# Kernel optimization log

Measured on AMD Instinct MI355X. Metric: run time of the kernel, lower is better.

Reference implementation:

```python
import jax, jax.numpy as jnp
import numpy as np

V = 1_000_000
D = 128
H = 128
DO = 128
S = 50_000


def setup_inputs() -> dict:
    key = jax.random.key(0)
    k1, k2, k3, k4, k5 = jax.random.split(key, 5)
    element_embeddings = jax.random.normal(k1, (V, D), dtype=jnp.float32)
    element_to_sample_map = jnp.sort(jax.random.randint(k2, (V,), 0, S))
    W_key = jax.random.normal(k3, (H, D), dtype=jnp.float32) * 0.05
    W_value = jax.random.normal(k4, (H, D), dtype=jnp.float32) * 0.05
    W_out = jax.random.normal(k5, (DO, D), dtype=jnp.float32) * 0.05
    return {
        "element_embeddings": element_embeddings,
        "element_to_sample_map": element_to_sample_map,
        "num_samples": S,
        "W_key": W_key,
        "W_value": W_value,
        "W_out": W_out,
    }


def _segment_log_softmax(scores, seg, num_segments):
    # numerically stable per-segment log-softmax (eps=0 as in original)
    m = jax.ops.segment_max(scores, seg, num_segments=num_segments)  # [S]
    m = jnp.where(jnp.isfinite(m), m, 0.0)  # guard empty segments
    shifted = scores - m[seg]
    sum_exp = jax.ops.segment_sum(jnp.exp(shifted), seg, num_segments=num_segments)  # [S]
    lse = jnp.log(sum_exp)
    return shifted - lse[seg]


def reference(element_embeddings, element_to_sample_map, num_samples, W_key, W_value, W_out):
    seg = element_to_sample_map
    # key summarizer: linear projection then per-sample mean (SimpleVarSizedElementReduce 'mean')
    proj = element_embeddings @ W_key.T  # [V, H]
    seg_sum = jax.ops.segment_sum(proj, seg, num_segments=num_samples)  # [S, H]
    counts = jax.ops.segment_sum(jnp.ones((proj.shape[0],), proj.dtype), seg, num_segments=num_samples)
    keys = seg_sum / jnp.maximum(counts, 1.0)[:, None]  # [S, H]

    keys_all = keys[seg]  # gather [V, H]
    values = element_embeddings @ W_value.T  # [V, H]
    attention_scores = jnp.einsum("vh,vh->v", keys_all, values)  # [V]
    attention_probs = jnp.exp(_segment_log_softmax(attention_scores, seg, num_samples))  # [V]

    out_vals = (element_embeddings @ W_out.T) * attention_probs[:, None]  # [V, DO]
    return jax.ops.segment_sum(out_vals, seg, num_segments=num_samples)  # [S, DO]
```

## Files before the change

### kernel.cpp

```cpp
#include <hip/hip_runtime.h>
#include <math.h>

#define G    4
#define CAP  104

typedef __attribute__((ext_vector_type(8))) short bf16x8;
typedef __attribute__((ext_vector_type(4))) float f32x4;

__global__ void k_segstarts(const int* __restrict__ map, int* __restrict__ starts,
                            int V, int S) {
    int i = blockIdx.x * blockDim.x + threadIdx.x;
    if (i >= V) return;
    int cur  = map[i];
    int prev = (i == 0) ? -1 : map[i - 1];
    for (int s = prev + 1; s <= cur; ++s) starts[s] = i;
    if (i == V - 1) {
        for (int s = cur + 1; s <= S; ++s) starts[s] = V;
    }
}

__device__ __forceinline__ unsigned f2bf_rte(float x) {
    unsigned b = __float_as_uint(x);
    b += 0x7FFFu + ((b >> 16) & 1u);
    return b >> 16;
}
__device__ __forceinline__ float bfu_lo(unsigned u) {
    return __uint_as_float(u << 16);
}
__device__ __forceinline__ float bfu_hi(unsigned u) {
    return __uint_as_float(u & 0xFFFF0000u);
}

template <int CTRL>
__device__ __forceinline__ float dpp_add(float v) {
    int t = __builtin_amdgcn_update_dpp(0, __float_as_int(v), CTRL, 0xF, 0xF, true);
    return v + __int_as_float(t);
}
__device__ __forceinline__ float red32_sum(float v) {
    v = dpp_add<0xB1>(v);
    v = dpp_add<0x4E>(v);
    v = dpp_add<0x141>(v);
    v = dpp_add<0x140>(v);
    v += __int_as_float(__builtin_amdgcn_ds_swizzle(__float_as_int(v), 0x401F));
    return v;
}

__global__ void k_prep(const float* __restrict__ Wk, const float* __restrict__ Wv,
                       const float* __restrict__ Wo,
                       unsigned short* __restrict__ Mpk,
                       unsigned short* __restrict__ Wpk) {
    const int i = blockIdx.x;
    const int j = threadIdx.x;
    float acc = 0.f;
#pragma unroll 8
    for (int h = 0; h < 128; ++h)
        acc += Wk[h * 128 + i] * Wv[h * 128 + j];
    acc *= 1.4426950408889634f;

    const int kt  = i >> 5;
    const int kg  = (i >> 3) & 3;
    const int t   = i & 7;
    const int jt  = j >> 4;
    const int l16 = j & 15;
    const int lane = kg * 16 + l16;
    const size_t idx = ((size_t)(kt * 8 + jt) * 64 + lane) * 8 + t;
    Mpk[idx] = (unsigned short)f2bf_rte(acc);
    Wpk[idx] = (unsigned short)f2bf_rte(Wo[j * 128 + i]);
}

__device__ __forceinline__ bf16x8 pack_a8(const float* p) {
    union { unsigned u[4]; bf16x8 v; } r;
    const float4 f0 = *(const float4*)p;
    const float4 f1 = *(const float4*)(p + 4);
    r.u[0] = (__float_as_uint(f0.y) & 0xFFFF0000u) | (__float_as_uint(f0.x) >> 16);
    r.u[1] = (__float_as_uint(f0.w) & 0xFFFF0000u) | (__float_as_uint(f0.z) >> 16);
    r.u[2] = (__float_as_uint(f1.y) & 0xFFFF0000u) | (__float_as_uint(f1.x) >> 16);
    r.u[3] = (__float_as_uint(f1.w) & 0xFFFF0000u) | (__float_as_uint(f1.z) >> 16);
    return r.v;
}

__global__ __launch_bounds__(256, 4) void k_main(
    const float* __restrict__ E, const int* __restrict__ starts,
    const unsigned short* __restrict__ Mpk, const unsigned short* __restrict__ Wpk,
    float* __restrict__ out, int V, int S)
{
    __shared__ unsigned sA[CAP][64];
    __shared__ float    sE[G][128];
    __shared__ float    sQ[G][128];

    const int tid  = threadIdx.x;
    const int w    = tid >> 6;
    const int lane = tid & 63;
    const int s0   = blockIdx.x * G;

    const int se    = min(s0 + G, S);
    const int gr0   = starts[s0];
    const int nrows = starts[se] - gr0;
    const bool staged = (nrows <= CAP);

    const int c  = lane & 31;
    const int g  = lane >> 5;

    if (staged && nrows > 0) {
        const int q4 = tid & 31;
        const int rr = tid >> 5;
        const float* gp = E + (size_t)gr0 * 128 + q4 * 4;
#pragma unroll
        for (int b = 0; b < 3; ++b) {
            const int nb = (b == 2) ? 3 : 5;
            const int k0 = b * 5;
            float4 t[5];
            for (int k = 0; k < nb; ++k) {
                const int r = min(rr + (k0 + k) * 8, nrows - 1);
                t[k] = *(const float4*)(gp + (size_t)r * 128);
            }
            for (int k = 0; k < nb; ++k) {
                uint2 u;
                u.x = f2bf_rte(t[k].x) | (f2bf_rte(t[k].y) << 16);
                u.y = f2bf_rte(t[k].z) | (f2bf_rte(t[k].w) << 16);
                *(uint2*)&sA[rr + (k0 + k) * 8][q4 * 2] = u;
            }
        }
    }
    __syncthreads();

    const int segi = s0 + w;
    int r0 = 0, n = 0, off = 0;
    if (segi < S) {
        r0  = starts[segi];
        n   = starts[segi + 1] - r0;
        off = r0 - gr0;
    }
    const int nfull = n & ~1;

    {
        float4 sum = make_float4(0.f, 0.f, 0.f, 0.f);
        if (segi < S && n > 0) {
            if (staged) {
                const unsigned* pA = &sA[off + g][c * 2];
                for (int rp = 0; rp < nfull; rp += 2) {
                    const uint2 u = *(const uint2*)pA;
                    pA += 128;
                    sum.x += bfu_lo(u.x); sum.y += bfu_hi(u.x);
                    sum.z += bfu_lo(u.y); sum.w += bfu_hi(u.y);
                }
                if ((n & 1) && g == 0) {
                    const uint2 u = *(const uint2*)&sA[off + n - 1][c * 2];
                    sum.x += bfu_lo(u.x); sum.y += bfu_hi(u.x);
                    sum.z += bfu_lo(u.y); sum.w += bfu_hi(u.y);
                }
            } else {
                const float* bp = E + (size_t)r0 * 128 + c * 4;
                for (int rp = 0; rp < nfull; rp += 2) {
                    const float4 ev = *(const float4*)(bp + (size_t)(rp + g) * 128);
                    sum.x += ev.x; sum.y += ev.y; sum.z += ev.z; sum.w += ev.w;
                }
                if ((n & 1) && g == 0) {
                    const float4 ev = *(const float4*)(bp + (size_t)(n - 1) * 128);
                    sum.x += ev.x; sum.y += ev.y; sum.z += ev.z; sum.w += ev.w;
                }
            }
            sum.x += __shfl_xor(sum.x, 32);
            sum.y += __shfl_xor(sum.y, 32);
            sum.z += __shfl_xor(sum.z, 32);
            sum.w += __shfl_xor(sum.w, 32);
            const float inv = 1.0f / (float)n;
            sum.x *= inv; sum.y *= inv; sum.z *= inv; sum.w *= inv;
        }
        if (g == 0)
            *(float4*)&sE[w][c * 4] = sum;
    }
    __syncthreads();

    const int arow = lane & 15;
    const int akg  = lane >> 4;
    {
        f32x4 c0 = {0.f, 0.f, 0.f, 0.f};
        f32x4 c1 = {0.f, 0.f, 0.f, 0.f};
        const uint4* Bp = (const uint4*)Mpk;
#pragma unroll
        for (int kt = 0; kt < 4; ++kt) {
            const bf16x8 a = pack_a8(&sE[arow & 3][kt * 32 + akg * 8]);
            union { uint4 u; bf16x8 v; } b0, b1;
            b0.u = Bp[(size_t)(kt * 8 + 2 * w) * 64 + lane];
            b1.u = Bp[(size_t)(kt * 8 + 2 * w + 1) * 64 + lane];
            c0 = __builtin_amdgcn_mfma_f32_16x16x32_bf16(a, b0.v, c0, 0, 0, 0);
            c1 = __builtin_amdgcn_mfma_f32_16x16x32_bf16(a, b1.v, c1, 0, 0, 0);
        }
        if (akg == 0) {
#pragma unroll
            for (int r = 0; r < 4; ++r) {
                sQ[r][(2 * w) * 16 + arow]     = c0[r];
                sQ[r][(2 * w + 1) * 16 + arow] = c1[r];
            }
        }
    }
    __syncthreads();

    {
        float4 acc = make_float4(0.f, 0.f, 0.f, 0.f);
        float Z = 0.f;
        if (segi < S && n > 0) {
            const float4 qv = *(const float4*)&sQ[w][c * 4];
            if (staged) {
                const unsigned* pA = &sA[off + g][c * 2];
                for (int rp = 0; rp < nfull; rp += 2) {
                    const uint2 u = *(const uint2*)pA;
                    pA += 128;
                    const float e0 = bfu_lo(u.x), e1 = bfu_hi(u.x);
                    const float e2 = bfu_lo(u.y), e3 = bfu_hi(u.y);
                    float pd = e0 * qv.x + e1 * qv.y + e2 * qv.z + e3 * qv.w;
                    pd = red32_sum(pd);
                    const float wgt = exp2f(pd);
                    Z += wgt;
                    acc.x += wgt * e0; acc.y += wgt * e1;
                    acc.z += wgt * e2; acc.w += wgt * e3;
                }
                if ((n & 1) && g == 0) {
                    const uint2 u = *(const uint2*)&sA[off + n - 1][c * 2];
                    const float e0 = bfu_lo(u.x), e1 = bfu_hi(u.x);
                    const float e2 = bfu_lo(u.y), e3 = bfu_hi(u.y);
                    float pd = e0 * qv.x + e1 * qv.y + e2 * qv.z + e3 * qv.w;
                    pd = red32_sum(pd);
                    const float wgt = exp2f(pd);
                    Z += wgt;
                    acc.x += wgt * e0; acc.y += wgt * e1;
                    acc.z += wgt * e2; acc.w += wgt * e3;
                }
            } else {
                const float* bp = E + (size_t)r0 * 128 + c * 4;
                for (int rp = 0; rp < nfull; rp += 2) {
                    const float4 ev = *(const float4*)(bp + (size_t)(rp + g) * 128);
                    float pd = ev.x * qv.x + ev.y * qv.y
                             + ev.z * qv.z + ev.w * qv.w;
                    pd = red32_sum(pd);
                    const float wgt = exp2f(pd);
                    Z += wgt;
                    acc.x += wgt * ev.x; acc.y += wgt * ev.y;
                    acc.z += wgt * ev.z; acc.w += wgt * ev.w;
                }
                if ((n & 1) && g == 0) {
                    const float4 ev = *(const float4*)(bp + (size_t)(n - 1) * 128);
                    float pd = ev.x * qv.x + ev.y * qv.y
                             + ev.z * qv.z + ev.w * qv.w;
                    pd = red32_sum(pd);
                    const float wgt = exp2f(pd);
                    Z += wgt;
                    acc.x += wgt * ev.x; acc.y += wgt * ev.y;
                    acc.z += wgt * ev.z; acc.w += wgt * ev.w;
                }
            }
            acc.x += __shfl_xor(acc.x, 32);
            acc.y += __shfl_xor(acc.y, 32);
            acc.z += __shfl_xor(acc.z, 32);
            acc.w += __shfl_xor(acc.w, 32);
            Z     += __shfl_xor(Z, 32);
            const float invZ = 1.0f / Z;
            acc.x *= invZ; acc.y *= invZ; acc.z *= invZ; acc.w *= invZ;
        }
        if (g == 0)
            *(float4*)&sE[w][c * 4] = acc;
    }
    __syncthreads();

    {
        f32x4 c0 = {0.f, 0.f, 0.f, 0.f};
        f32x4 c1 = {0.f, 0.f, 0.f, 0.f};
        const uint4* Bp = (const uint4*)Wpk;
#pragma unroll
        for (int kt = 0; kt < 4; ++kt) {
            const bf16x8 a = pack_a8(&sE[arow & 3][kt * 32 + akg * 8]);
            union { uint4 u; bf16x8 v; } b0, b1;
            b0.u = Bp[(size_t)(kt * 8 + 2 * w) * 64 + lane];
            b1.u = Bp[(size_t)(kt * 8 + 2 * w + 1) * 64 + lane];
            c0 = __builtin_amdgcn_mfma_f32_16x16x32_bf16(a, b0.v, c0, 0, 0, 0);
            c1 = __builtin_amdgcn_mfma_f32_16x16x32_bf16(a, b1.v, c1, 0, 0, 0);
        }
        if (akg == 0) {
#pragma unroll
            for (int r = 0; r < 4; ++r) {
                const int s = s0 + r;
                if (s < S) {
                    out[(size_t)s * 128 + (2 * w) * 16 + arow]     = c0[r];
                    out[(size_t)s * 128 + (2 * w + 1) * 16 + arow] = c1[r];
                }
            }
        }
    }
}

extern "C" void kernel_launch(void* const* d_in, const int* in_sizes, int n_in,
                              void* d_out, int out_size, void* d_ws, size_t ws_size,
                              hipStream_t stream) {
    const float* E   = (const float*)d_in[0];
    const int*   map = (const int*)d_in[1];
    const float* Wk  = (const float*)d_in[3];
    const float* Wv  = (const float*)d_in[4];
    const float* Wo  = (const float*)d_in[5];
    float* out = (float*)d_out;

    const int V = in_sizes[1];
    const int S = out_size / 128;

    char* p = (char*)d_ws;
    auto alloc = [&](size_t b) {
        char* r = p;
        p += (b + 255) & ~(size_t)255;
        return r;
    };
    int*            starts = (int*)alloc((size_t)(S + 1) * sizeof(int));
    unsigned short* Mpk    = (unsigned short*)alloc(128 * 128 * sizeof(unsigned short));
    unsigned short* Wpk    = (unsigned short*)alloc(128 * 128 * sizeof(unsigned short));

    k_segstarts<<<(V + 255) / 256, 256, 0, stream>>>(map, starts, V, S);
    k_prep<<<128, 128, 0, stream>>>(Wk, Wv, Wo, Mpk, Wpk);
    k_main<<<(S + G - 1) / G, 256, 0, stream>>>(E, starts, Mpk, Wpk, out, V, S);
}
```

Measured before the change: 137.9 us.

## Compute staged attention scores with MFMA and swizzle shared bf16 tile

```diff
diff --git a/kernel.cpp b/kernel.cpp
--- a/kernel.cpp
+++ b/kernel.cpp
@@ -3,6 +3,7 @@
 
 #define G    4
 #define CAP  104
+#define SROW 112
 
 typedef __attribute__((ext_vector_type(8))) short bf16x8;
 typedef __attribute__((ext_vector_type(4))) float f32x4;
@@ -79,14 +80,19 @@
     return r.v;
 }
 
+__device__ __forceinline__ int swz(int row, int uoff) {
+    return uoff ^ ((row & 7) << 2);
+}
+
 __global__ __launch_bounds__(256, 4) void k_main(
     const float* __restrict__ E, const int* __restrict__ starts,
     const unsigned short* __restrict__ Mpk, const unsigned short* __restrict__ Wpk,
     float* __restrict__ out, int V, int S)
 {
-    __shared__ unsigned sA[CAP][64];
+    __shared__ unsigned sA[SROW][64];
     __shared__ float    sE[G][128];
     __shared__ float    sQ[G][128];
+    __shared__ float    sS[G][SROW];
 
     const int tid  = threadIdx.x;
     const int w    = tid >> 6;
@@ -115,10 +121,11 @@
                 t[k] = *(const float4*)(gp + (size_t)r * 128);
             }
             for (int k = 0; k < nb; ++k) {
+                const int row = rr + (k0 + k) * 8;
                 uint2 u;
                 u.x = f2bf_rte(t[k].x) | (f2bf_rte(t[k].y) << 16);
                 u.y = f2bf_rte(t[k].z) | (f2bf_rte(t[k].w) << 16);
-                *(uint2*)&sA[rr + (k0 + k) * 8][q4 * 2] = u;
+                *(uint2*)&sA[row][swz(row, q4 * 2)] = u;
             }
         }
     }
@@ -137,15 +144,15 @@
         float4 sum = make_float4(0.f, 0.f, 0.f, 0.f);
         if (segi < S && n > 0) {
             if (staged) {
-                const unsigned* pA = &sA[off + g][c * 2];
                 for (int rp = 0; rp < nfull; rp += 2) {
-                    const uint2 u = *(const uint2*)pA;
-                    pA += 128;
+                    const int row = off + rp + g;
+                    const uint2 u = *(const uint2*)&sA[row][swz(row, c * 2)];
                     sum.x += bfu_lo(u.x); sum.y += bfu_hi(u.x);
                     sum.z += bfu_lo(u.y); sum.w += bfu_hi(u.y);
                 }
                 if ((n & 1) && g == 0) {
-                    const uint2 u = *(const uint2*)&sA[off + n - 1][c * 2];
+                    const int row = off + n - 1;
+                    const uint2 u = *(const uint2*)&sA[row][swz(row, c * 2)];
                     sum.x += bfu_lo(u.x); sum.y += bfu_hi(u.x);
                     sum.z += bfu_lo(u.y); sum.w += bfu_hi(u.y);
                 }
@@ -197,58 +204,90 @@
     }
     __syncthreads();
 
-    {
+    if (staged) {
+        {
+            const int Tall = (nrows + 15) >> 4;
+            bf16x8 bq[4];
+#pragma unroll
+            for (int kt = 0; kt < 4; ++kt)
+                bq[kt] = pack_a8(&sQ[arow & 3][kt * 32 + akg * 8]);
+            for (int t = w; t < Tall; t += 4) {
+                const int rbase = t * 16 + arow;
+                f32x4 cs = {0.f, 0.f, 0.f, 0.f};
+#pragma unroll
+                for (int kt = 0; kt < 4; ++kt) {
+                    union { uint4 u; bf16x8 v; } a;
+                    a.u = *(const uint4*)&sA[rbase][swz(rbase, kt * 16 + akg * 4)];
+                    cs = __builtin_amdgcn_mfma_f32_16x16x32_bf16(a.v, bq[kt], cs, 0, 0, 0);
+                }
+                if (arow < 4) {
+#pragma unroll
+                    for (int r = 0; r < 4; ++r)
+                        sS[arow][t * 16 + akg * 4 + r] = cs[r];
+                }
+            }
+        }
+        __syncthreads();
+
+        for (int i = tid; i < G * SROW; i += 256) {
+            sS[0][i] = exp2f(sS[0][i]);
+        }
+        __syncthreads();
+
+        {
+            float4 acc = make_float4(0.f, 0.f, 0.f, 0.f);
+            float Z = 0.f;
+            if (segi < S && n > 0) {
+                for (int rp = 0; rp < nfull; rp += 2) {
+                    const int row = off + rp + g;
+                    const uint2 u = *(const uint2*)&sA[row][swz(row, c * 2)];
+                    const float wgt = sS[w][row];
+                    Z += wgt;
+                    acc.x += wgt * bfu_lo(u.x); acc.y += wgt * bfu_hi(u.x);
+                    acc.z += wgt * bfu_lo(u.y); acc.w += wgt * bfu_hi(u.y);
+                }
+                if ((n & 1) && g == 0) {
+                    const int row = off + n - 1;
+                    const uint2 u = *(const uint2*)&sA[row][swz(row, c * 2)];
+                    const float wgt = sS[w][row];
+                    Z += wgt;
+                    acc.x += wgt * bfu_lo(u.x); acc.y += wgt * bfu_hi(u.x);
+                    acc.z += wgt * bfu_lo(u.y); acc.w += wgt * bfu_hi(u.y);
+                }
+                acc.x += __shfl_xor(acc.x, 32);
+                acc.y += __shfl_xor(acc.y, 32);
+                acc.z += __shfl_xor(acc.z, 32);
+                acc.w += __shfl_xor(acc.w, 32);
+                Z     += __shfl_xor(Z, 32);
+                const float invZ = 1.0f / Z;
+                acc.x *= invZ; acc.y *= invZ; acc.z *= invZ; acc.w *= invZ;
+            }
+            if (g == 0)
+                *(float4*)&sE[w][c * 4] = acc;
+        }
+    } else {
         float4 acc = make_float4(0.f, 0.f, 0.f, 0.f);
         float Z = 0.f;
         if (segi < S && n > 0) {
             const float4 qv = *(const float4*)&sQ[w][c * 4];
-            if (staged) {
-                const unsigned* pA = &sA[off + g][c * 2];
-                for (int rp = 0; rp < nfull; rp += 2) {
-                    const uint2 u = *(const uint2*)pA;
-                    pA += 128;
-                    const float e0 = bfu_lo(u.x), e1 = bfu_hi(u.x);
-                    const float e2 = bfu_lo(u.y), e3 = bfu_hi(u.y);
-                    float pd = e0 * qv.x + e1 * qv.y + e2 * qv.z + e3 * qv.w;
-                    pd = red32_sum(pd);
-                    const float wgt = exp2f(pd);
-                    Z += wgt;
-                    acc.x += wgt * e0; acc.y += wgt * e1;
-                    acc.z += wgt * e2; acc.w += wgt * e3;
-                }
-                if ((n & 1) && g == 0) {
-                    const uint2 u = *(const uint2*)&sA[off + n - 1][c * 2];
-                    const float e0 = bfu_lo(u.x), e1 = bfu_hi(u.x);
-                    const float e2 = bfu_lo(u.y), e3 = bfu_hi(u.y);
-                    float pd = e0 * qv.x + e1 * qv.y + e2 * qv.z + e3 * qv.w;
-                    pd = red32_sum(pd);
-                    const float wgt = exp2f(pd);
-                    Z += wgt;
-                    acc.x += wgt * e0; acc.y += wgt * e1;
-                    acc.z += wgt * e2; acc.w += wgt * e3;
-                }
-            } else {
-                const float* bp = E + (size_t)r0 * 128 + c * 4;
-                for (int rp = 0; rp < nfull; rp += 2) {
-                    const float4 ev = *(const float4*)(bp + (size_t)(rp + g) * 128);
-                    float pd = ev.x * qv.x + ev.y * qv.y
-                             + ev.z * qv.z + ev.w * qv.w;
-                    pd = red32_sum(pd);
-                    const float wgt = exp2f(pd);
-                    Z += wgt;
-                    acc.x += wgt * ev.x; acc.y += wgt * ev.y;
-                    acc.z += wgt * ev.z; acc.w += wgt * ev.w;
-                }
-                if ((n & 1) && g == 0) {
-                    const float4 ev = *(const float4*)(bp + (size_t)(n - 1) * 128);
-                    float pd = ev.x * qv.x + ev.y * qv.y
-                             + ev.z * qv.z + ev.w * qv.w;
-                    pd = red32_sum(pd);
-                    const float wgt = exp2f(pd);
-                    Z += wgt;
-                    acc.x += wgt * ev.x; acc.y += wgt * ev.y;
-                    acc.z += wgt * ev.z; acc.w += wgt * ev.w;
-                }
+            const float* bp = E + (size_t)r0 * 128 + c * 4;
+            for (int rp = 0; rp < nfull; rp += 2) {
+                const float4 ev = *(const float4*)(bp + (size_t)(rp + g) * 128);
+                float pd = ev.x * qv.x + ev.y * qv.y + ev.z * qv.z + ev.w * qv.w;
+                pd = red32_sum(pd);
+                const float wgt = exp2f(pd);
+                Z += wgt;
+                acc.x += wgt * ev.x; acc.y += wgt * ev.y;
+                acc.z += wgt * ev.z; acc.w += wgt * ev.w;
+            }
+            if ((n & 1) && g == 0) {
+                const float4 ev = *(const float4*)(bp + (size_t)(n - 1) * 128);
+                float pd = ev.x * qv.x + ev.y * qv.y + ev.z * qv.z + ev.w * qv.w;
+                pd = red32_sum(pd);
+                const float wgt = exp2f(pd);
+                Z += wgt;
+                acc.x += wgt * ev.x; acc.y += wgt * ev.y;
+                acc.z += wgt * ev.z; acc.w += wgt * ev.w;
             }
             acc.x += __shfl_xor(acc.x, 32);
             acc.y += __shfl_xor(acc.y, 32);
```

After: 145.1 us. +5.2%, slower.
